# Kernel optimization log

Measured on AMD Instinct MI355X. Metric: run time of the kernel, lower is better.

The kernel has to match this reference:

```python
import jax, jax.numpy as jnp
import numpy as np

NBX = 24  # nb_x_patches
NBY = 24  # nb_y_patches
B, H, D = 8, 12, 64
L = NBX * NBY + 1  # 577 (grid tokens + 1 CLS token from the pad)
EPS = 1e-08


def _toeplitz_mask(topological_params):
    # topological_params: [H, 4*NBX*NBY]
    gi = jnp.arange(NBX)
    gj = jnp.arange(NBY)
    # relative 2D displacement index, flattened over (i, j, i', j')
    dist_index = ((gi[:, None, None, None] - gi[None, None, :, None] + NBX) * 2 * NBY
                  + gj[None, :, None, None] - gj[None, None, None, :] + NBY)
    dist_index = dist_index.reshape(-1)
    m = jnp.take(topological_params, dist_index, axis=1)
    m = m.reshape(topological_params.shape[0], NBX * NBY, NBX * NBY)  # [H, L-1, L-1]
    # pad CLS row and column with 1.0
    m = jnp.pad(m, [[0, 0], [1, 0], [1, 0]], constant_values=1.0)  # [H, L, L]
    return m[None]  # [1, H, L, L]


def setup_inputs() -> dict:
    key = jax.random.key(0)
    k1, k2, k3, k4 = jax.random.split(key, 4)
    return {
        'query': jax.random.normal(k1, (B, L, H, D), dtype=jnp.float32),
        'key': jax.random.normal(k2, (B, L, H, D), dtype=jnp.float32),
        'value': jax.random.normal(k3, (B, L, H, D), dtype=jnp.float32),
        'topological_params': jax.random.normal(k4, (H, 4 * NBX * NBY), dtype=jnp.float32),
    }


def reference(query, key, value, topological_params):
    depth = query.shape[-1]
    q = query / jnp.sqrt(jnp.asarray(depth, query.dtype))
    # relu feature map (kernel_type == 'relu')
    q = jax.nn.relu(q) + EPS
    k = jax.nn.relu(key) + EPS
    attn = jnp.einsum('bqhd,bkhd->bhqk', q, k)  # [B, H, L, L]
    top_mask = _toeplitz_mask(topological_params)  # [1, H, L, L]
    attn = attn * jnp.abs(top_mask) + EPS
    attn = attn / jnp.sum(attn, axis=-1, keepdims=True)  # kernelized normalization (no softmax)
    return jnp.einsum('bhqk,bkhd->bqhd', attn, value)
```

## Files before the change

kernel.cpp:

```cpp
#include <hip/hip_runtime.h>


#define Lq 577
#define NH 12
#define NB 8
#define DD 64
#define PAR 2304
#define EPSf 1e-8f

#define VT_OFF 7090176ull
#define M2_OFF 14954496ull

#define KBLK 1731
#define VBLK 960
#define MBLK 480

typedef __attribute__((ext_vector_type(4))) float f32x4;
typedef __attribute__((ext_vector_type(8))) short s16x8;

__device__ __forceinline__ float bflo(unsigned int u) {
    return __builtin_bit_cast(float, u << 16);
}
__device__ __forceinline__ float bfhi(unsigned int u) {
    return __builtin_bit_cast(float, u & 0xffff0000u);
}
__device__ __forceinline__ unsigned int f2bf(float f) {
    unsigned int x = __builtin_bit_cast(unsigned int, f);
    return (x + 0x7fffu + ((x >> 16) & 1u)) >> 16;
}
__device__ __forceinline__ int imin(int a, int b) { return a < b ? a : b; }

__device__ __forceinline__ void gload_lds16(const unsigned short* g, unsigned short* l) {
    __builtin_amdgcn_global_load_lds(
        (const __attribute__((address_space(1))) unsigned int*)g,
        (__attribute__((address_space(3))) unsigned int*)l, 16, 0, 0);
}

__device__ __forceinline__ bool probe_f32(const void* Qg) {
    float x = fabsf(((const float*)Qg)[threadIdx.x]);
    unsigned long long hit = __ballot(x > 2.44140625e-4f && x < 64.0f);
    unsigned long long act = __ballot(1);
    return 2 * __popcll(hit) >= __popcll(act);
}

template <bool F32>
__device__ __forceinline__ void load8f(const void* G, size_t eidx, float* o) {
    if constexpr (F32) {
        const float* p = (const float*)G + eidx;
        float4 a = *(const float4*)p;
        float4 b = *(const float4*)(p + 4);
        o[0] = a.x; o[1] = a.y; o[2] = a.z; o[3] = a.w;
        o[4] = b.x; o[5] = b.y; o[6] = b.z; o[7] = b.w;
    } else {
        const unsigned short* p = (const unsigned short*)G + eidx;
        uint4 a = *(const uint4*)p;
        unsigned int u[4] = {a.x, a.y, a.z, a.w};
#pragma unroll
        for (int j = 0; j < 4; ++j) {
            o[2 * j]     = bflo(u[j]);
            o[2 * j + 1] = bfhi(u[j]);
        }
    }
}

template <bool F32>
__device__ void prep_k_body(const void* Kg, unsigned short* Kp, int bx) {
    size_t i8 = ((size_t)bx * 256 + threadIdx.x) * 8;
    float f[8];
    load8f<F32>(Kg, i8, f);
    unsigned int o[4];
#pragma unroll
    for (int j = 0; j < 4; ++j) {
        unsigned int lo = f2bf(fmaxf(f[2 * j], 0.0f) + EPSf);
        unsigned int hi = f2bf(fmaxf(f[2 * j + 1], 0.0f) + EPSf);
        o[j] = lo | (hi << 16);
    }
    *(uint4*)(Kp + i8) = make_uint4(o[0], o[1], o[2], o[3]);
}

template <bool F32>
__device__ void prep_vt_body(const void* Vg, unsigned short* Vt,
                             unsigned short* s, int id) {
    const int t  = threadIdx.x;
    const int kt = id % 10;
    const int h  = (id / 10) % NH;
    const int b  = id / 120;
    {
        int kl  = t >> 2;
        int dch = (t & 3) * 16;
        int k   = kt * 64 + kl;
        unsigned int pk[8] = {};
        if (k <= 576) {
            float f[16];
            size_t base = ((size_t)((b * Lq + k) * NH + h)) * DD + dch;
            load8f<F32>(Vg, base, f);
            load8f<F32>(Vg, base + 8, f + 8);
#pragma unroll
            for (int j = 0; j < 8; ++j) {
                float a0 = f[2 * j], a1 = f[2 * j + 1];
                a0 = (a0 == a0) ? a0 : 0.0f;
                a1 = (a1 == a1) ? a1 : 0.0f;
                pk[j] = f2bf(a0) | (f2bf(a1) << 16);
            }
        }
#pragma unroll
        for (int j = 0; j < 8; ++j)
            *(unsigned int*)&s[kl * 72 + dch + 2 * j] = pk[j];
    }
    __syncthreads();
    {
        int d   = t >> 2;
        int kch = (t & 3) * 16;
        unsigned int o[8];
#pragma unroll
        for (int j = 0; j < 8; ++j) {
            unsigned short v0 = s[(kch + 2 * j) * 72 + d];
            unsigned short v1 = s[(kch + 2 * j + 1) * 72 + d];
            o[j] = (unsigned int)v0 | ((unsigned int)v1 << 16);
        }
        size_t base = ((size_t)((b * NH + h) * 64 + d)) * 640 + kt * 64 + kch;
        *(uint4*)(Vt + base)     = make_uint4(o[0], o[1], o[2], o[3]);
        *(uint4*)(Vt + base + 8) = make_uint4(o[4], o[5], o[6], o[7]);
    }
}

template <bool F32>
__device__ void prep_m2_body(const void* Tg, unsigned short* M2, int id) {
    const int qg = id % 40;
    const int h  = id / 40;
    const int t    = threadIdx.x;
    const int cf   = t >> 6;
    const int lane = t & 63;
    const int lm   = lane & 15;
    const int g    = lane >> 4;
    const int q    = qg * 16 + lm;
    const bool qok = q < Lq;
    int cq = 0;
    if (qok && q > 0) {
        int qq = q - 1;
        int qi = (qq * 2731) >> 16;
        cq = qq + 24 * qi + 1176;
    }
    for (int kt = 0; kt < 10; ++kt) {
        unsigned int hv[4];
#pragma unroll
        for (int e = 0; e < 4; ++e) {
            int k = kt * 64 + cf * 16 + g * 4 + e;
            float m;
            if (!qok || k > 576) m = 0.0f;
            else if (k == 0 || q == 0) m = 1.0f;
            else {
                int kk = k - 1;
                int ki = (kk * 2731) >> 16;
                int idx = cq - (kk + 24 * ki);
                float pv = F32 ? ((const float*)Tg)[h * PAR + idx]
                               : bflo((unsigned int)((const unsigned short*)Tg)[h * PAR + idx]);
                m = fabsf(pv);
                m = (m == m) ? m : 0.0f;
            }
            hv[e] = f2bf(m);
        }
        size_t base = ((size_t)(((h * 40 + qg) * 10 + kt) * 4 + cf) * 64 + lane) * 4;
        *(uint2*)(M2 + base) = make_uint2(hv[0] | (hv[1] << 16), hv[2] | (hv[3] << 16));
    }
}

__global__ __launch_bounds__(256)
void prep_all(const void* __restrict__ Qg, const void* __restrict__ Kg,
              const void* __restrict__ Vg, const void* __restrict__ Tg,
              unsigned short* __restrict__ Kp, unsigned short* __restrict__ Vt,
              unsigned short* __restrict__ M2) {
    __shared__ unsigned short s[64 * 72];
    bool f32 = probe_f32(Qg);
    int bx = blockIdx.x;
    if (bx < KBLK) {
        if (f32) prep_k_body<true>(Kg, Kp, bx);
        else     prep_k_body<false>(Kg, Kp, bx);
    } else if (bx < KBLK + VBLK) {
        if (f32) prep_vt_body<true>(Vg, Vt, s, bx - KBLK);
        else     prep_vt_body<false>(Vg, Vt, s, bx - KBLK);
    } else {
        if (f32) prep_m2_body<true>(Tg, M2, bx - KBLK - VBLK);
        else     prep_m2_body<false>(Tg, M2, bx - KBLK - VBLK);
    }
}

template <bool F32>
__device__ void attn_body(const void* __restrict__ Qg,
                          const unsigned short* __restrict__ Kp,
                          const unsigned short* __restrict__ Vt,
                          const unsigned short* __restrict__ M2,
                          void* __restrict__ Og,
                          unsigned short* s_k, unsigned short* s_vt,
                          unsigned short* s_p_all) {
    const int tid  = threadIdx.x;
    const int w    = tid >> 6;
    const int lane = tid & 63;
    const int g    = lane >> 4;
    const int lm   = lane & 15;

    const int bid = blockIdx.x;
    const int qt  = bid / 96;
    const int bh  = bid - qt * 96;
    const int h   = bh % NH;
    const int b   = bh / NH;

    unsigned short* s_pw = s_p_all + w * 16 * 72;

    const int q0w = qt * 64 + w * 16;
    const int qg  = qt * 4 + w;

    const int q  = q0w + lm;
    const int qc = imin(q, Lq - 1);
    s16x8 a_q[2];
    {
        size_t rbase = ((size_t)((b * Lq + qc) * NH + h)) * DD;
#pragma unroll
        for (int ds = 0; ds < 2; ++ds) {
            float f[8];
            load8f<F32>(Qg, rbase + ds * 32 + g * 8, f);
            s16x8 a;
#pragma unroll
            for (int j = 0; j < 8; ++j) {
                float v = fmaf(fmaxf(f[j], 0.0f), 0.125f, EPSf);
                a[j] = (short)f2bf(v);
            }
            a_q[ds] = a;
        }
    }

    const int r8 = lane >> 3;
    const int c8 = lane & 7;
    const int xr = (c8 ^ r8) * 8;
    const int x7 = lm & 7;

    const unsigned short* KpBH = Kp + (size_t)b * (Lq * NH * DD) + h * DD;
    const unsigned short* VtL0 = Vt + ((size_t)(b * NH + h) * 64 + (w * 16 + r8)) * 640 + xr;
    const unsigned short* Mw   = M2 + (size_t)(h * 40 + qg) * 10240 + lane * 4;

    f32x4 o_acc[4] = {};
    float rs = 0.0f;

    uint2 mcur[4], mnxt[4];

    auto stage = [&](int t, int buf) {
        int kbn = t * 64;
        int krr = kbn + w * 16 + r8;
        int kr0 = imin(krr, Lq - 1);
        int kr1 = imin(krr + 8, Lq - 1);
        unsigned short* k0 = s_k  + buf * 4096 + (w * 16) * 64;
        unsigned short* v0 = s_vt + buf * 4096 + (w * 16) * 64;
        gload_lds16(KpBH + (size_t)kr0 * (NH * DD) + xr, k0);
        gload_lds16(KpBH + (size_t)kr1 * (NH * DD) + xr, k0 + 512);
        gload_lds16(VtL0 + kbn, v0);
        gload_lds16(VtL0 + 8 * 640 + kbn, v0 + 512);
    };

    stage(0, 0);
#pragma unroll
    for (int cf = 0; cf < 4; ++cf) mcur[cf] = *(const uint2*)(Mw + cf * 256);

#pragma unroll 2
    for (int t = 0; t < 10; ++t) {
        const int cur = t & 1;
        __syncthreads();

        if (t < 9) {
            stage(t + 1, cur ^ 1);
#pragma unroll
            for (int cf = 0; cf < 4; ++cf)
                mnxt[cf] = *(const uint2*)(Mw + (t + 1) * 1024 + cf * 256);
        }

        const unsigned short* skb = s_k  + cur * 4096;
        const unsigned short* svb = s_vt + cur * 4096;

        f32x4 sf[4];
#pragma unroll
        for (int cf = 0; cf < 4; ++cf) {
            const unsigned short* skr = skb + (cf * 16 + lm) * 64;
            int co = (g ^ x7) * 8;
            s16x8 kf0 = *(const s16x8*)(skr + co);
            s16x8 kf1 = *(const s16x8*)(skr + (co ^ 32));
            f32x4 acc = {};
            acc = __builtin_amdgcn_mfma_f32_16x16x32_bf16(kf0, a_q[0], acc, 0, 0, 0);
            acc = __builtin_amdgcn_mfma_f32_16x16x32_bf16(kf1, a_q[1], acc, 0, 0, 0);
            sf[cf] = acc;
        }

#pragma unroll
        for (int cf = 0; cf < 4; ++cf) {
            float m0 = bflo(mcur[cf].x), m1 = bfhi(mcur[cf].x);
            float m2 = bflo(mcur[cf].y), m3 = bfhi(mcur[cf].y);
            float p0 = fmaf(fmaxf(sf[cf][0], 0.0f), m0, EPSf);
            float p1 = fmaf(fmaxf(sf[cf][1], 0.0f), m1, EPSf);
            float p2 = fmaf(fmaxf(sf[cf][2], 0.0f), m2, EPSf);
            float p3 = fmaf(fmaxf(sf[cf][3], 0.0f), m3, EPSf);
            rs += (p0 + p1) + (p2 + p3);
            unsigned int d0 = f2bf(p0) | (f2bf(p1) << 16);
            unsigned int d1 = f2bf(p2) | (f2bf(p3) << 16);
            *(uint2*)&s_pw[lm * 72 + cf * 16 + g * 4] = make_uint2(d0, d1);
        }

#pragma unroll
        for (int ks = 0; ks < 2; ++ks) {
            s16x8 pa = *(const s16x8*)&s_pw[lm * 72 + ks * 32 + g * 8];
#pragma unroll
            for (int df = 0; df < 4; ++df) {
                const unsigned short* svr = svb + (df * 16 + lm) * 64;
                s16x8 vb = *(const s16x8*)(svr + ((ks * 4 + g) ^ x7) * 8);
                o_acc[df] = __builtin_amdgcn_mfma_f32_16x16x32_bf16(pa, vb, o_acc[df], 0, 0, 0);
            }
        }

#pragma unroll
        for (int cf = 0; cf < 4; ++cf) mcur[cf] = mnxt[cf];
    }

    float tot = rs;
    tot += __shfl_xor(tot, 16, 64);
    tot += __shfl_xor(tot, 32, 64);
    float inv = (tot > 0.0f) ? 1.0f / tot : 0.0f;

#pragma unroll
    for (int r = 0; r < 4; ++r) {
        int   qrow  = q0w + g * 4 + r;
        float inv_r = __shfl(inv, g * 4 + r, 64);
        if (qrow < Lq) {
            size_t base = ((size_t)((b * Lq + qrow) * NH + h)) * DD;
#pragma unroll
            for (int df = 0; df < 4; ++df) {
                float val = o_acc[df][r] * inv_r;
                if constexpr (F32)
                    ((float*)Og)[base + df * 16 + lm] = val;
                else
                    ((unsigned short*)Og)[base + df * 16 + lm] = (unsigned short)f2bf(val);
            }
        }
    }
}

__global__ __launch_bounds__(256, 3)
void fused_topo_attn(const void* __restrict__ Qg,
                     const unsigned short* __restrict__ Kp,
                     const unsigned short* __restrict__ Vt,
                     const unsigned short* __restrict__ M2,
                     void* __restrict__ Og) {
    __shared__ __align__(16) unsigned short s_k[2 * 64 * 64];
    __shared__ __align__(16) unsigned short s_vt[2 * 64 * 64];
    __shared__ __align__(16) unsigned short s_p[4 * 16 * 72];

    if (probe_f32(Qg)) attn_body<true>(Qg, Kp, Vt, M2, Og, s_k, s_vt, s_p);
    else               attn_body<false>(Qg, Kp, Vt, M2, Og, s_k, s_vt, s_p);
}

extern "C" void kernel_launch(void* const* d_in, const int* in_sizes, int n_in,
                              void* d_out, int out_size, void* d_ws, size_t ws_size,
                              hipStream_t stream) {
    (void)in_sizes; (void)n_in; (void)out_size; (void)ws_size;
    unsigned short* Kp = (unsigned short*)d_ws;
    unsigned short* Vt = (unsigned short*)((char*)d_ws + VT_OFF);
    unsigned short* M2 = (unsigned short*)((char*)d_ws + M2_OFF);

    prep_all<<<KBLK + VBLK + MBLK, 256, 0, stream>>>(
        d_in[0], d_in[1], d_in[2], d_in[3], Kp, Vt, M2);
    fused_topo_attn<<<960, 256, 0, stream>>>(d_in[0], Kp, Vt, M2, d_out);
}
```

Before: 125.5 us.

## Load K/V fragments directly from global into registers, drop LDS staging

```diff
diff --git a/kernel.cpp b/kernel.cpp
--- a/kernel.cpp
+++ b/kernel.cpp
@@ -29,12 +29,6 @@
     return (x + 0x7fffu + ((x >> 16) & 1u)) >> 16;
 }
 __device__ __forceinline__ int imin(int a, int b) { return a < b ? a : b; }
-
-__device__ __forceinline__ void gload_lds16(const unsigned short* g, unsigned short* l) {
-    __builtin_amdgcn_global_load_lds(
-        (const __attribute__((address_space(1))) unsigned int*)g,
-        (__attribute__((address_space(3))) unsigned int*)l, 16, 0, 0);
-}
 
 __device__ __forceinline__ bool probe_f32(const void* Qg) {
     float x = fabsf(((const float*)Qg)[threadIdx.x]);
@@ -191,7 +185,6 @@
                           const unsigned short* __restrict__ Vt,
                           const unsigned short* __restrict__ M2,
                           void* __restrict__ Og,
-                          unsigned short* s_k, unsigned short* s_vt,
                           unsigned short* s_p_all) {
     const int tid  = threadIdx.x;
     const int w    = tid >> 6;
@@ -229,69 +222,52 @@
         }
     }
 
-    const int r8 = lane >> 3;
-    const int c8 = lane & 7;
-    const int xr = (c8 ^ r8) * 8;
-    const int x7 = lm & 7;
-
-    const unsigned short* KpBH = Kp + (size_t)b * (Lq * NH * DD) + h * DD;
-    const unsigned short* VtL0 = Vt + ((size_t)(b * NH + h) * 64 + (w * 16 + r8)) * 640 + xr;
-    const unsigned short* Mw   = M2 + (size_t)(h * 40 + qg) * 10240 + lane * 4;
+    const unsigned short* KpBH = Kp + (size_t)b * (Lq * NH * DD) + h * DD + g * 8;
+    const unsigned short* VtD[4];
+#pragma unroll
+    for (int df = 0; df < 4; ++df)
+        VtD[df] = Vt + ((size_t)(b * NH + h) * 64 + (df * 16 + lm)) * 640 + g * 8;
+    const unsigned short* Mw = M2 + (size_t)(h * 40 + qg) * 10240 + lane * 4;
 
     f32x4 o_acc[4] = {};
     float rs = 0.0f;
 
-    uint2 mcur[4], mnxt[4];
-
-    auto stage = [&](int t, int buf) {
-        int kbn = t * 64;
-        int krr = kbn + w * 16 + r8;
-        int kr0 = imin(krr, Lq - 1);
-        int kr1 = imin(krr + 8, Lq - 1);
-        unsigned short* k0 = s_k  + buf * 4096 + (w * 16) * 64;
-        unsigned short* v0 = s_vt + buf * 4096 + (w * 16) * 64;
-        gload_lds16(KpBH + (size_t)kr0 * (NH * DD) + xr, k0);
-        gload_lds16(KpBH + (size_t)kr1 * (NH * DD) + xr, k0 + 512);
-        gload_lds16(VtL0 + kbn, v0);
-        gload_lds16(VtL0 + 8 * 640 + kbn, v0 + 512);
-    };
-
-    stage(0, 0);
-#pragma unroll
-    for (int cf = 0; cf < 4; ++cf) mcur[cf] = *(const uint2*)(Mw + cf * 256);
-
-#pragma unroll 2
+#pragma unroll 1
     for (int t = 0; t < 10; ++t) {
-        const int cur = t & 1;
-        __syncthreads();
-
-        if (t < 9) {
-            stage(t + 1, cur ^ 1);
-#pragma unroll
-            for (int cf = 0; cf < 4; ++cf)
-                mnxt[cf] = *(const uint2*)(Mw + (t + 1) * 1024 + cf * 256);
-        }
-
-        const unsigned short* skb = s_k  + cur * 4096;
-        const unsigned short* svb = s_vt + cur * 4096;
+        const int kb = t * 64;
+
+        s16x8 kf[4][2];
+#pragma unroll
+        for (int cf = 0; cf < 4; ++cf) {
+            int krow = imin(kb + cf * 16 + lm, Lq - 1);
+            const unsigned short* kp = KpBH + (size_t)krow * (NH * DD);
+            kf[cf][0] = *(const s16x8*)kp;
+            kf[cf][1] = *(const s16x8*)(kp + 32);
+        }
+        s16x8 vf[2][4];
+#pragma unroll
+        for (int ks = 0; ks < 2; ++ks)
+#pragma unroll
+            for (int df = 0; df < 4; ++df)
+                vf[ks][df] = *(const s16x8*)(VtD[df] + kb + ks * 32);
+        uint2 mu[4];
+#pragma unroll
+        for (int cf = 0; cf < 4; ++cf)
+            mu[cf] = *(const uint2*)(Mw + t * 1024 + cf * 256);
 
         f32x4 sf[4];
 #pragma unroll
         for (int cf = 0; cf < 4; ++cf) {
-            const unsigned short* skr = skb + (cf * 16 + lm) * 64;
-            int co = (g ^ x7) * 8;
-            s16x8 kf0 = *(const s16x8*)(skr + co);
-            s16x8 kf1 = *(const s16x8*)(skr + (co ^ 32));
             f32x4 acc = {};
-            acc = __builtin_amdgcn_mfma_f32_16x16x32_bf16(kf0, a_q[0], acc, 0, 0, 0);
-            acc = __builtin_amdgcn_mfma_f32_16x16x32_bf16(kf1, a_q[1], acc, 0, 0, 0);
+            acc = __builtin_amdgcn_mfma_f32_16x16x32_bf16(kf[cf][0], a_q[0], acc, 0, 0, 0);
+            acc = __builtin_amdgcn_mfma_f32_16x16x32_bf16(kf[cf][1], a_q[1], acc, 0, 0, 0);
             sf[cf] = acc;
         }
 
 #pragma unroll
         for (int cf = 0; cf < 4; ++cf) {
-            float m0 = bflo(mcur[cf].x), m1 = bfhi(mcur[cf].x);
-            float m2 = bflo(mcur[cf].y), m3 = bfhi(mcur[cf].y);
+            float m0 = bflo(mu[cf].x), m1 = bfhi(mu[cf].x);
+            float m2 = bflo(mu[cf].y), m3 = bfhi(mu[cf].y);
             float p0 = fmaf(fmaxf(sf[cf][0], 0.0f), m0, EPSf);
             float p1 = fmaf(fmaxf(sf[cf][1], 0.0f), m1, EPSf);
             float p2 = fmaf(fmaxf(sf[cf][2], 0.0f), m2, EPSf);
@@ -306,15 +282,10 @@
         for (int ks = 0; ks < 2; ++ks) {
             s16x8 pa = *(const s16x8*)&s_pw[lm * 72 + ks * 32 + g * 8];
 #pragma unroll
-            for (int df = 0; df < 4; ++df) {
-                const unsigned short* svr = svb + (df * 16 + lm) * 64;
-                s16x8 vb = *(const s16x8*)(svr + ((ks * 4 + g) ^ x7) * 8);
-                o_acc[df] = __builtin_amdgcn_mfma_f32_16x16x32_bf16(pa, vb, o_acc[df], 0, 0, 0);
-            }
-        }
-
-#pragma unroll
-        for (int cf = 0; cf < 4; ++cf) mcur[cf] = mnxt[cf];
+            for (int df = 0; df < 4; ++df)
+                o_acc[df] = __builtin_amdgcn_mfma_f32_16x16x32_bf16(pa, vf[ks][df],
+                                                                    o_acc[df], 0, 0, 0);
+        }
     }
 
     float tot = rs;
@@ -346,12 +317,10 @@
                      const unsigned short* __restrict__ Vt,
                      const unsigned short* __restrict__ M2,
                      void* __restrict__ Og) {
-    __shared__ __align__(16) unsigned short s_k[2 * 64 * 64];
-    __shared__ __align__(16) unsigned short s_vt[2 * 64 * 64];
     __shared__ __align__(16) unsigned short s_p[4 * 16 * 72];
 
-    if (probe_f32(Qg)) attn_body<true>(Qg, Kp, Vt, M2, Og, s_k, s_vt, s_p);
-    else               attn_body<false>(Qg, Kp, Vt, M2, Og, s_k, s_vt, s_p);
+    if (probe_f32(Qg)) attn_body<true>(Qg, Kp, Vt, M2, Og, s_p);
+    else               attn_body<false>(Qg, Kp, Vt, M2, Og, s_p);
 }
 
 extern "C" void kernel_launch(void* const* d_in, const int* in_sizes, int n_in,
```

Result: slower. 173.4 us (+38.2%).

## Give each wave two query subtiles with half the waves per block

Applied to the files above, without the earlier changes.

```diff
diff --git a/kernel.cpp b/kernel.cpp
--- a/kernel.cpp
+++ b/kernel.cpp
@@ -192,7 +192,7 @@
                           const unsigned short* __restrict__ M2,
                           void* __restrict__ Og,
                           unsigned short* s_k, unsigned short* s_vt,
-                          unsigned short* s_p_all) {
+                          unsigned short* s_p) {
     const int tid  = threadIdx.x;
     const int w    = tid >> 6;
     const int lane = tid & 63;
@@ -205,15 +205,14 @@
     const int h   = bh % NH;
     const int b   = bh / NH;
 
-    unsigned short* s_pw = s_p_all + w * 16 * 72;
-
-    const int q0w = qt * 64 + w * 16;
-    const int qg  = qt * 4 + w;
-
-    const int q  = q0w + lm;
-    const int qc = imin(q, Lq - 1);
-    s16x8 a_q[2];
-    {
+    unsigned short* s_pw = s_p + w * 2048;
+
+    const int q0w = qt * 64 + w * 32;
+
+    s16x8 a_q[2][2];
+#pragma unroll
+    for (int s = 0; s < 2; ++s) {
+        int qc = imin(q0w + s * 16 + lm, Lq - 1);
         size_t rbase = ((size_t)((b * Lq + qc) * NH + h)) * DD;
 #pragma unroll
         for (int ds = 0; ds < 2; ++ds) {
@@ -225,7 +224,7 @@
                 float v = fmaf(fmaxf(f[j], 0.0f), 0.125f, EPSf);
                 a[j] = (short)f2bf(v);
             }
-            a_q[ds] = a;
+            a_q[s][ds] = a;
         }
     }
 
@@ -235,30 +234,34 @@
     const int x7 = lm & 7;
 
     const unsigned short* KpBH = Kp + (size_t)b * (Lq * NH * DD) + h * DD;
-    const unsigned short* VtL0 = Vt + ((size_t)(b * NH + h) * 64 + (w * 16 + r8)) * 640 + xr;
-    const unsigned short* Mw   = M2 + (size_t)(h * 40 + qg) * 10240 + lane * 4;
-
-    f32x4 o_acc[4] = {};
-    float rs = 0.0f;
-
-    uint2 mcur[4], mnxt[4];
+    const unsigned short* VtBH = Vt + (size_t)(b * NH + h) * 64 * 640;
+    const unsigned short* Mw0  = M2 + (size_t)(h * 40 + qt * 4 + w * 2) * 10240 + lane * 4;
+    const unsigned short* Mw1  = Mw0 + 10240;
+
+    f32x4 o_acc[2][4] = {};
+    float rs[2] = {};
+
+    uint2 mcur[2][4], mnxt[2][4];
 
     auto stage = [&](int t, int buf) {
         int kbn = t * 64;
-        int krr = kbn + w * 16 + r8;
-        int kr0 = imin(krr, Lq - 1);
-        int kr1 = imin(krr + 8, Lq - 1);
-        unsigned short* k0 = s_k  + buf * 4096 + (w * 16) * 64;
-        unsigned short* v0 = s_vt + buf * 4096 + (w * 16) * 64;
-        gload_lds16(KpBH + (size_t)kr0 * (NH * DD) + xr, k0);
-        gload_lds16(KpBH + (size_t)kr1 * (NH * DD) + xr, k0 + 512);
-        gload_lds16(VtL0 + kbn, v0);
-        gload_lds16(VtL0 + 8 * 640 + kbn, v0 + 512);
+#pragma unroll
+        for (int i = 0; i < 4; ++i) {
+            int krow = imin(kbn + w * 32 + i * 8 + r8, Lq - 1);
+            int drow = w * 32 + i * 8 + r8;
+            unsigned short* kd = s_k  + buf * 4096 + (w * 32 + i * 8) * 64;
+            unsigned short* vd = s_vt + buf * 4096 + (w * 32 + i * 8) * 64;
+            gload_lds16(KpBH + (size_t)krow * (NH * DD) + xr, kd);
+            gload_lds16(VtBH + (size_t)drow * 640 + kbn + xr, vd);
+        }
     };
 
     stage(0, 0);
 #pragma unroll
-    for (int cf = 0; cf < 4; ++cf) mcur[cf] = *(const uint2*)(Mw + cf * 256);
+    for (int cf = 0; cf < 4; ++cf) {
+        mcur[0][cf] = *(const uint2*)(Mw0 + cf * 256);
+        mcur[1][cf] = *(const uint2*)(Mw1 + cf * 256);
+    }
 
 #pragma unroll 2
     for (int t = 0; t < 10; ++t) {
@@ -268,79 +271,95 @@
         if (t < 9) {
             stage(t + 1, cur ^ 1);
 #pragma unroll
-            for (int cf = 0; cf < 4; ++cf)
-                mnxt[cf] = *(const uint2*)(Mw + (t + 1) * 1024 + cf * 256);
+            for (int cf = 0; cf < 4; ++cf) {
+                mnxt[0][cf] = *(const uint2*)(Mw0 + (t + 1) * 1024 + cf * 256);
+                mnxt[1][cf] = *(const uint2*)(Mw1 + (t + 1) * 1024 + cf * 256);
+            }
         }
 
         const unsigned short* skb = s_k  + cur * 4096;
         const unsigned short* svb = s_vt + cur * 4096;
 
-        f32x4 sf[4];
+        f32x4 sf[2][4];
 #pragma unroll
         for (int cf = 0; cf < 4; ++cf) {
             const unsigned short* skr = skb + (cf * 16 + lm) * 64;
             int co = (g ^ x7) * 8;
             s16x8 kf0 = *(const s16x8*)(skr + co);
             s16x8 kf1 = *(const s16x8*)(skr + (co ^ 32));
-            f32x4 acc = {};
-            acc = __builtin_amdgcn_mfma_f32_16x16x32_bf16(kf0, a_q[0], acc, 0, 0, 0);
-            acc = __builtin_amdgcn_mfma_f32_16x16x32_bf16(kf1, a_q[1], acc, 0, 0, 0);
-            sf[cf] = acc;
-        }
-
-#pragma unroll
-        for (int cf = 0; cf < 4; ++cf) {
-            float m0 = bflo(mcur[cf].x), m1 = bfhi(mcur[cf].x);
-            float m2 = bflo(mcur[cf].y), m3 = bfhi(mcur[cf].y);
-            float p0 = fmaf(fmaxf(sf[cf][0], 0.0f), m0, EPSf);
-            float p1 = fmaf(fmaxf(sf[cf][1], 0.0f), m1, EPSf);
-            float p2 = fmaf(fmaxf(sf[cf][2], 0.0f), m2, EPSf);
-            float p3 = fmaf(fmaxf(sf[cf][3], 0.0f), m3, EPSf);
-            rs += (p0 + p1) + (p2 + p3);
-            unsigned int d0 = f2bf(p0) | (f2bf(p1) << 16);
-            unsigned int d1 = f2bf(p2) | (f2bf(p3) << 16);
-            *(uint2*)&s_pw[lm * 72 + cf * 16 + g * 4] = make_uint2(d0, d1);
-        }
+#pragma unroll
+            for (int s = 0; s < 2; ++s) {
+                f32x4 acc = {};
+                acc = __builtin_amdgcn_mfma_f32_16x16x32_bf16(kf0, a_q[s][0], acc, 0, 0, 0);
+                acc = __builtin_amdgcn_mfma_f32_16x16x32_bf16(kf1, a_q[s][1], acc, 0, 0, 0);
+                sf[s][cf] = acc;
+            }
+        }
+
+#pragma unroll
+        for (int s = 0; s < 2; ++s)
+#pragma unroll
+            for (int cf = 0; cf < 4; ++cf) {
+                float m0 = bflo(mcur[s][cf].x), m1 = bfhi(mcur[s][cf].x);
+                float m2 = bflo(mcur[s][cf].y), m3 = bfhi(mcur[s][cf].y);
+                float p0 = fmaf(fmaxf(sf[s][cf][0], 0.0f), m0, EPSf);
+                float p1 = fmaf(fmaxf(sf[s][cf][1], 0.0f), m1, EPSf);
+                float p2 = fmaf(fmaxf(sf[s][cf][2], 0.0f), m2, EPSf);
+                float p3 = fmaf(fmaxf(sf[s][cf][3], 0.0f), m3, EPSf);
+                rs[s] += (p0 + p1) + (p2 + p3);
+                unsigned int d0 = f2bf(p0) | (f2bf(p1) << 16);
+                unsigned int d1 = f2bf(p2) | (f2bf(p3) << 16);
+                int col = ((cf * 2 + (g >> 1)) ^ x7) * 8 + (g & 1) * 4;
+                *(uint2*)&s_pw[(s * 16 + lm) * 64 + col] = make_uint2(d0, d1);
+            }
 
 #pragma unroll
         for (int ks = 0; ks < 2; ++ks) {
-            s16x8 pa = *(const s16x8*)&s_pw[lm * 72 + ks * 32 + g * 8];
+            s16x8 pa[2];
+#pragma unroll
+            for (int s = 0; s < 2; ++s)
+                pa[s] = *(const s16x8*)&s_pw[(s * 16 + lm) * 64 + ((ks * 4 + g) ^ x7) * 8];
 #pragma unroll
             for (int df = 0; df < 4; ++df) {
                 const unsigned short* svr = svb + (df * 16 + lm) * 64;
                 s16x8 vb = *(const s16x8*)(svr + ((ks * 4 + g) ^ x7) * 8);
-                o_acc[df] = __builtin_amdgcn_mfma_f32_16x16x32_bf16(pa, vb, o_acc[df], 0, 0, 0);
-            }
-        }
-
-#pragma unroll
-        for (int cf = 0; cf < 4; ++cf) mcur[cf] = mnxt[cf];
-    }
-
-    float tot = rs;
-    tot += __shfl_xor(tot, 16, 64);
-    tot += __shfl_xor(tot, 32, 64);
-    float inv = (tot > 0.0f) ? 1.0f / tot : 0.0f;
-
-#pragma unroll
-    for (int r = 0; r < 4; ++r) {
-        int   qrow  = q0w + g * 4 + r;
-        float inv_r = __shfl(inv, g * 4 + r, 64);
-        if (qrow < Lq) {
-            size_t base = ((size_t)((b * Lq + qrow) * NH + h)) * DD;
-#pragma unroll
-            for (int df = 0; df < 4; ++df) {
-                float val = o_acc[df][r] * inv_r;
-                if constexpr (F32)
-                    ((float*)Og)[base + df * 16 + lm] = val;
-                else
-                    ((unsigned short*)Og)[base + df * 16 + lm] = (unsigned short)f2bf(val);
-            }
-        }
-    }
-}
-
-__global__ __launch_bounds__(256, 3)
+                o_acc[0][df] = __builtin_amdgcn_mfma_f32_16x16x32_bf16(pa[0], vb, o_acc[0][df], 0, 0, 0);
+                o_acc[1][df] = __builtin_amdgcn_mfma_f32_16x16x32_bf16(pa[1], vb, o_acc[1][df], 0, 0, 0);
+            }
+        }
+
+#pragma unroll
+        for (int s = 0; s < 2; ++s)
+#pragma unroll
+            for (int cf = 0; cf < 4; ++cf) mcur[s][cf] = mnxt[s][cf];
+    }
+
+#pragma unroll
+    for (int s = 0; s < 2; ++s) {
+        float tot = rs[s];
+        tot += __shfl_xor(tot, 16, 64);
+        tot += __shfl_xor(tot, 32, 64);
+        float inv = (tot > 0.0f) ? 1.0f / tot : 0.0f;
+#pragma unroll
+        for (int r = 0; r < 4; ++r) {
+            int   qrow  = q0w + s * 16 + g * 4 + r;
+            float inv_r = __shfl(inv, g * 4 + r, 64);
+            if (qrow < Lq) {
+                size_t base = ((size_t)((b * Lq + qrow) * NH + h)) * DD;
+#pragma unroll
+                for (int df = 0; df < 4; ++df) {
+                    float val = o_acc[s][df][r] * inv_r;
+                    if constexpr (F32)
+                        ((float*)Og)[base + df * 16 + lm] = val;
+                    else
+                        ((unsigned short*)Og)[base + df * 16 + lm] = (unsigned short)f2bf(val);
+                }
+            }
+        }
+    }
+}
+
+__global__ __launch_bounds__(128, 2)
 void fused_topo_attn(const void* __restrict__ Qg,
                      const unsigned short* __restrict__ Kp,
                      const unsigned short* __restrict__ Vt,
@@ -348,7 +367,7 @@
                      void* __restrict__ Og) {
     __shared__ __align__(16) unsigned short s_k[2 * 64 * 64];
     __shared__ __align__(16) unsigned short s_vt[2 * 64 * 64];
-    __shared__ __align__(16) unsigned short s_p[4 * 16 * 72];
+    __shared__ __align__(16) unsigned short s_p[2 * 32 * 64];
 
     if (probe_f32(Qg)) attn_body<true>(Qg, Kp, Vt, M2, Og, s_k, s_vt, s_p);
     else               attn_body<false>(Qg, Kp, Vt, M2, Og, s_k, s_vt, s_p);
@@ -364,5 +383,5 @@
 
     prep_all<<<KBLK + VBLK + MBLK, 256, 0, stream>>>(
         d_in[0], d_in[1], d_in[2], d_in[3], Kp, Vt, M2);
-    fused_topo_attn<<<960, 256, 0, stream>>>(d_in[0], Kp, Vt, M2, d_out);
-}
+    fused_topo_attn<<<960, 128, 0, stream>>>(d_in[0], Kp, Vt, M2, d_out);
+}
```

After: 123.6 us. Within noise of the previous version (-1.5%).
